# Performance work log

Measured on AMD Instinct MI355X. Metric: run time of the kernel, lower is better.

## Reference

```python
import jax, jax.numpy as jnp
import numpy as np

EMB = 1024
HID = 4 * EMB
HEADS = 16
HEAD_DIM = EMB // HEADS


def gelu_tanh(x):
    c = jnp.sqrt(jnp.asarray(2.0 / jnp.pi, x.dtype))
    return 0.5 * x * (1.0 + jnp.tanh(c * (x + 0.044715 * x ** 3)))


def layernorm(x, scale, shift, eps=1e-5):
    mean = jnp.mean(x, axis=-1, keepdims=True)
    var = jnp.var(x, axis=-1, keepdims=True)
    return scale * (x - mean) / jnp.sqrt(var + eps) + shift


def setup_inputs() -> dict:
    key = jax.random.key(0)
    ks = jax.random.split(key, 12)
    s = 0.02
    return {
        "x": jax.random.normal(ks[0], (2, 2048, EMB), jnp.float32),
        "Wq": jax.random.normal(ks[1], (EMB, EMB), jnp.float32) * s,
        "Wk": jax.random.normal(ks[2], (EMB, EMB), jnp.float32) * s,
        "Wv": jax.random.normal(ks[3], (EMB, EMB), jnp.float32) * s,
        "Wo": jax.random.normal(ks[4], (EMB, EMB), jnp.float32) * s,
        "bo": jnp.zeros((EMB,), jnp.float32),
        "W1": jax.random.normal(ks[5], (EMB, HID), jnp.float32) * s,
        "b1": jnp.zeros((HID,), jnp.float32),
        "W2": jax.random.normal(ks[6], (HID, EMB), jnp.float32) * s,
        "b2": jnp.zeros((EMB,), jnp.float32),
        "ln1_scale": jnp.ones((EMB,), jnp.float32),
        "ln1_shift": jnp.zeros((EMB,), jnp.float32),
        "ln2_scale": jnp.ones((EMB,), jnp.float32),
        "ln2_shift": jnp.zeros((EMB,), jnp.float32),
    }


def reference(x, Wq, Wk, Wv, Wo, bo, W1, b1, W2, b2,
              ln1_scale, ln1_shift, ln2_scale, ln2_shift):
    B, S, D = x.shape

    # pre-norm attention + residual
    h = layernorm(x, ln1_scale, ln1_shift)
    q = (h @ Wq).reshape(B, S, HEADS, HEAD_DIM).transpose(0, 2, 1, 3)  # bhsd
    k = (h @ Wk).reshape(B, S, HEADS, HEAD_DIM).transpose(0, 2, 1, 3)
    v = (h @ Wv).reshape(B, S, HEADS, HEAD_DIM).transpose(0, 2, 1, 3)

    scores = jnp.einsum("bhqd,bhkd->bhqk", q, k)
    causal = jnp.tril(jnp.ones((S, S), bool))
    scores = jnp.where(causal, scores, -jnp.inf)
    attn = jax.nn.softmax(scores / jnp.sqrt(jnp.asarray(HEAD_DIM, x.dtype)), axis=-1)
    ctx = jnp.einsum("bhqk,bhkd->bhqd", attn, v)
    ctx = ctx.transpose(0, 2, 1, 3).reshape(B, S, D)
    x = x + (ctx @ Wo + bo)

    # pre-norm FFN + residual
    h = layernorm(x, ln2_scale, ln2_shift)
    h = gelu_tanh(h @ W1 + b1) @ W2 + b2
    return x + h
```

## Files before the change

kernel.cpp:

```cpp
#include <hip/hip_runtime.h>
#include <hip/hip_bf16.h>
#include <stdint.h>

#define B_   2
#define S_   2048
#define D_   1024
#define H_   16
#define DH_  64
#define HID_ 4096
#define M_   4096

typedef __bf16 bf16x8 __attribute__((ext_vector_type(8)));
typedef float  f32x4  __attribute__((ext_vector_type(4)));
typedef float  f32x16 __attribute__((ext_vector_type(16)));
typedef uint32_t u32x4v __attribute__((ext_vector_type(4)));

typedef const uint32_t __attribute__((address_space(1))) u32g;
typedef uint32_t       __attribute__((address_space(3))) u32l;

#define SCL2K_ 0.18033688011112042f

__device__ __forceinline__ uint16_t f2bf(float f) {
  uint32_t u = __builtin_bit_cast(uint32_t, f);
  u += 0x7FFFu + ((u >> 16) & 1u);
  return (uint16_t)(u >> 16);
}

__device__ __forceinline__ float bf2f(uint16_t u) {
  return __builtin_bit_cast(float, (uint32_t)u << 16);
}

__device__ __forceinline__ void gload_lds16(const void* g, void* l) {
  __builtin_amdgcn_global_load_lds((u32g*)g, (u32l*)l, 16, 0, 0);
}

__device__ __forceinline__ const bf16x8* lds8p(const uint16_t* base, int row,
                                               int cole) {
  int byt = (cole * 2) ^ ((row & 7) << 4);
  return reinterpret_cast<const bf16x8*>(base + row * 64 + (byt >> 1));
}

__device__ __forceinline__ const bf16x8* lds8p32(const uint16_t* base, int row,
                                                 int cole) {
  int byt = (cole * 2) ^ ((row & 7) << 4) ^ ((row & 8) << 2);
  return reinterpret_cast<const bf16x8*>(base + row * 64 + (byt >> 1));
}

__device__ __forceinline__ uint32_t cvtpk_bf16(float lo, float hi) {
  uint32_t d;
  asm("v_cvt_pk_bf16_f32 %0, %1, %2" : "=v"(d) : "v"(lo), "v"(hi));
  return d;
}
__device__ __forceinline__ void pl32swap(uint32_t& a, uint32_t& b) {
  asm volatile("v_permlane32_swap_b32 %0, %1" : "+v"(a), "+v"(b));
}

__global__ void prep_k(const float* __restrict__ Wq, const float* __restrict__ Wk,
                       const float* __restrict__ Wv, const float* __restrict__ Wo,
                       const float* __restrict__ W1, const float* __restrict__ W2,
                       uint16_t* __restrict__ WQKVT, uint16_t* __restrict__ WOT,
                       uint16_t* __restrict__ W1T, uint16_t* __restrict__ W2T,
                       const float* __restrict__ x, const float* __restrict__ sc,
                       const float* __restrict__ sh, uint16_t* __restrict__ lnout) {
  int idx = blockIdx.x;
  int tx = threadIdx.x, ty = threadIdx.y;
  if (idx >= 12288) {
    int row = idx - 12288;
    int t = ty * 32 + tx;
    float4 v = reinterpret_cast<const float4*>(x + (size_t)row * D_)[t];
    float s = v.x + v.y + v.z + v.w;
    float ss = v.x * v.x + v.y * v.y + v.z * v.z + v.w * v.w;
#pragma unroll
    for (int off = 32; off >= 1; off >>= 1) {
      s += __shfl_xor(s, off);
      ss += __shfl_xor(ss, off);
    }
    __shared__ float red[8];
    int wid = t >> 6, lane = t & 63;
    if (lane == 0) { red[wid] = s; red[wid + 4] = ss; }
    __syncthreads();
    s = red[0] + red[1] + red[2] + red[3];
    ss = red[4] + red[5] + red[6] + red[7];
    float mean = s * (1.0f / D_);
    float var = ss * (1.0f / D_) - mean * mean;
    float rstd = rsqrtf(var + 1e-5f);
    float4 g = reinterpret_cast<const float4*>(sc)[t];
    float4 b = reinterpret_cast<const float4*>(sh)[t];
    ushort4 o;
    o.x = f2bf(g.x * (v.x - mean) * rstd + b.x);
    o.y = f2bf(g.y * (v.y - mean) * rstd + b.y);
    o.z = f2bf(g.z * (v.z - mean) * rstd + b.z);
    o.w = f2bf(g.w * (v.w - mean) * rstd + b.w);
    reinterpret_cast<ushort4*>(lnout + (size_t)row * D_)[t] = o;
    return;
  }
  __shared__ float tile[32][33];
  const float* W;
  uint16_t* WT;
  int K, N, within;
  if (idx < 4096) {
    int which = idx >> 10;
    within = idx & 1023;
    W = (which == 0) ? Wq : (which == 1) ? Wk : (which == 2) ? Wv : Wo;
    WT = (which == 3) ? WOT : WQKVT + (size_t)which * 1024 * 1024;
    K = 1024; N = 1024;
  } else if (idx < 8192) {
    within = idx - 4096; W = W1; WT = W1T; K = 1024; N = 4096;
  } else {
    within = idx - 8192; W = W2; WT = W2T; K = 4096; N = 1024;
  }
  int nb = N >> 5;
  int n0 = (within % nb) * 32, k0 = (within / nb) * 32;
#pragma unroll
  for (int i = 0; i < 4; ++i)
    tile[ty + i * 8][tx] = W[(size_t)(k0 + ty + i * 8) * N + n0 + tx];
  __syncthreads();
#pragma unroll
  for (int i = 0; i < 4; ++i)
    WT[(size_t)(n0 + ty + i * 8) * K + k0 + tx] = f2bf(tile[tx][ty + i * 8]);
}

__global__ __launch_bounds__(256) void ln_k(const float* __restrict__ x,
                                            const float* __restrict__ sc,
                                            const float* __restrict__ sh,
                                            uint16_t* __restrict__ out) {
  int row = blockIdx.x;
  int t = threadIdx.x;
  float4 v = reinterpret_cast<const float4*>(x + (size_t)row * D_)[t];
  float s = v.x + v.y + v.z + v.w;
  float ss = v.x * v.x + v.y * v.y + v.z * v.z + v.w * v.w;
#pragma unroll
  for (int off = 32; off >= 1; off >>= 1) {
    s += __shfl_xor(s, off);
    ss += __shfl_xor(ss, off);
  }
  __shared__ float red[8];
  int wid = t >> 6, lane = t & 63;
  if (lane == 0) { red[wid] = s; red[wid + 4] = ss; }
  __syncthreads();
  s = red[0] + red[1] + red[2] + red[3];
  ss = red[4] + red[5] + red[6] + red[7];
  float mean = s * (1.0f / D_);
  float var = ss * (1.0f / D_) - mean * mean;
  float rstd = rsqrtf(var + 1e-5f);
  float4 g = reinterpret_cast<const float4*>(sc)[t];
  float4 b = reinterpret_cast<const float4*>(sh)[t];
  ushort4 o;
  o.x = f2bf(g.x * (v.x - mean) * rstd + b.x);
  o.y = f2bf(g.y * (v.y - mean) * rstd + b.y);
  o.z = f2bf(g.z * (v.z - mean) * rstd + b.z);
  o.w = f2bf(g.w * (v.w - mean) * rstd + b.w);
  reinterpret_cast<ushort4*>(out + (size_t)row * D_)[t] = o;
}

__global__ __launch_bounds__(256) void reduce4_k(
    const uint16_t* __restrict__ P0, const uint16_t* __restrict__ P1,
    const uint16_t* __restrict__ P2, const uint16_t* __restrict__ P3,
    const float* __restrict__ resid, const float* __restrict__ bias,
    float* __restrict__ out) {
  int row = blockIdx.x, t = threadIdx.x;
  size_t base = (size_t)row * D_ + t * 4;
  float4 r = *reinterpret_cast<const float4*>(resid + base);
  float4 b = reinterpret_cast<const float4*>(bias)[t];
  ushort4 u0 = *reinterpret_cast<const ushort4*>(P0 + base);
  ushort4 u1 = *reinterpret_cast<const ushort4*>(P1 + base);
  ushort4 u2 = *reinterpret_cast<const ushort4*>(P2 + base);
  ushort4 u3 = *reinterpret_cast<const ushort4*>(P3 + base);
  float4 o;
  o.x = r.x + b.x + bf2f(u0.x) + bf2f(u1.x) + bf2f(u2.x) + bf2f(u3.x);
  o.y = r.y + b.y + bf2f(u0.y) + bf2f(u1.y) + bf2f(u2.y) + bf2f(u3.y);
  o.z = r.z + b.z + bf2f(u0.z) + bf2f(u1.z) + bf2f(u2.z) + bf2f(u3.z);
  o.w = r.w + b.w + bf2f(u0.w) + bf2f(u1.w) + bf2f(u2.w) + bf2f(u3.w);
  *reinterpret_cast<float4*>(out + base) = o;
}

template <int EPI>
__global__ __launch_bounds__(512, 2) void gemm8(
    const uint16_t* __restrict__ A, const uint16_t* __restrict__ BT,
    void* __restrict__ Cout, const float* __restrict__ bias,
    uint16_t* __restrict__ P0, uint16_t* __restrict__ P1,
    uint16_t* __restrict__ P2, uint16_t* __restrict__ P3,
    int M, int N, int K) {
  __shared__ uint16_t As[2][2][128 * 64];
  __shared__ uint16_t Bs[2][2][128 * 64];
  int t = threadIdx.x;
  int lane = t & 63, wid = t >> 6;
  int wm = wid >> 2, wn = wid & 3;
  int l15 = lane & 15, lk8 = (lane >> 4) * 8, lr4 = (lane >> 4) * 4;
  int gx = gridDim.x;
  int nwg = gx * gridDim.y;
  int bid = blockIdx.y * gx + blockIdx.x;
  int swz = (bid & 7) * (nwg >> 3) + (bid >> 3);
  int bx = swz % gx, by = swz / gx;
  int m0 = by * 256, n0 = bx * 256;
  int ksz = K / gridDim.z;
  int kbeg = blockIdx.z * ksz;
  int NT = ksz >> 6;

  int r0 = t >> 3, slot0 = t & 7;
  int scol = (slot0 ^ (r0 & 7)) * 8;

  auto STAGE_A = [&](int kt, int half, int buf) {
    const uint16_t* src =
        A + (size_t)(m0 + half * 128 + r0) * K + kbeg + kt * 64 + scol;
    uint16_t* dst = &As[buf][half][t * 8];
    gload_lds16(src, dst);
    gload_lds16(src + (size_t)64 * K, dst + 4096);
  };
  auto STAGE_B = [&](int kt, int half, int buf) {
    const uint16_t* src =
        BT + (size_t)(n0 + half * 128 + r0) * K + kbeg + kt * 64 + scol;
    uint16_t* dst = &Bs[buf][half][t * 8];
    gload_lds16(src, dst);
    gload_lds16(src + (size_t)64 * K, dst + 4096);
  };

  bf16x8 a[4][2], b[2][2];
  auto LDA = [&](int buf, int mh) {
#pragma unroll
    for (int j = 0; j < 4; ++j)
#pragma unroll
      for (int kk = 0; kk < 2; ++kk)
        a[j][kk] = *lds8p(As[buf][mh], wm * 64 + j * 16 + l15, kk * 32 + lk8);
  };
  auto LDB = [&](int buf, int nh) {
#pragma unroll
    for (int jj = 0; jj < 2; ++jj)
#pragma unroll
      for (int kk = 0; kk < 2; ++kk)
        b[jj][kk] = *lds8p(Bs[buf][nh], wn * 32 + jj * 16 + l15, kk * 32 + lk8);
  };

  f32x4 acc[8][4] = {};
  auto MM = [&](int mh, int nh) {
    __builtin_amdgcn_s_setprio(1);
#pragma unroll
    for (int kk = 0; kk < 2; ++kk)
#pragma unroll
      for (int j = 0; j < 4; ++j)
#pragma unroll
        for (int jj = 0; jj < 2; ++jj)
          acc[mh * 4 + j][nh * 2 + jj] = __builtin_amdgcn_mfma_f32_16x16x32_bf16(
              a[j][kk], b[jj][kk], acc[mh * 4 + j][nh * 2 + jj], 0, 0, 0);
    __builtin_amdgcn_s_setprio(0);
  };
  auto BAR = [&]() { __builtin_amdgcn_s_barrier(); };

  STAGE_A(0, 0, 0);
  STAGE_B(0, 1, 0);
  STAGE_B(0, 0, 0);
  STAGE_A(0, 1, 0);
  STAGE_A(1, 0, 1);
  STAGE_B(1, 1, 1);
  asm volatile("s_waitcnt vmcnt(4)" ::: "memory");
  BAR();

  for (int T = 0; T < NT; ++T) {
    int cur = T & 1;
    LDA(cur, 0);
    LDB(cur, 0);
    if (T + 1 < NT) STAGE_B(T + 1, 0, cur ^ 1);
    BAR();
    MM(0, 0);
    BAR();
    LDB(cur, 1);
    if (T + 1 < NT) STAGE_A(T + 1, 1, cur ^ 1);
    BAR();
    MM(0, 1);
    BAR();
    LDA(cur, 1);
    if (T + 2 < NT) STAGE_A(T + 2, 0, cur);
    BAR();
    MM(1, 1);
    BAR();
    LDB(cur, 0);
    if (T + 2 < NT) STAGE_B(T + 2, 1, cur);
    BAR();
    MM(1, 0);
    if (T + 1 < NT) {
      if (T == NT - 2) {
        asm volatile("s_waitcnt vmcnt(0)" ::: "memory");
      } else {
        asm volatile("s_waitcnt vmcnt(4)" ::: "memory");
      }
    }
    BAR();
  }

  uint16_t* Pz = nullptr;
  if constexpr (EPI == 3) {
    int z = blockIdx.z;
    Pz = (z == 0) ? P0 : (z == 1) ? P1 : (z == 2) ? P2 : P3;
  }
#pragma unroll
  for (int mi = 0; mi < 8; ++mi) {
#pragma unroll
    for (int ni = 0; ni < 4; ++ni) {
      int gm0 = m0 + (mi >> 2) * 128 + wm * 64 + (mi & 3) * 16 + lr4;
      int gn = n0 + (ni >> 1) * 128 + wn * 32 + (ni & 1) * 16 + l15;
      if constexpr (EPI == 0) {
        int which = gn >> 10, nc = gn & 1023;
        int h = nc >> 6, dh = nc & 63;
        int bb = gm0 >> 11, s0 = gm0 & 2047;
        if (which == 2) {
          ushort4 vs;
          vs.x = f2bf(acc[mi][ni][0]);
          vs.y = f2bf(acc[mi][ni][1]);
          vs.z = f2bf(acc[mi][ni][2]);
          vs.w = f2bf(acc[mi][ni][3]);
          uint16_t* VTb = P0;
          *reinterpret_cast<ushort4*>(
              VTb + ((size_t)(bb * 16 + h) * 64 + dh) * S_ + s0) = vs;
        } else {
#pragma unroll
          for (int rr = 0; rr < 4; ++rr) {
            float v = acc[mi][ni][rr];
            if (which == 1) v *= SCL2K_;
            ((uint16_t*)Cout)[((size_t)which * 32 + bb * 16 + h) * (S_ * 64) +
                              (size_t)(s0 + rr) * 64 + dh] = f2bf(v);
          }
        }
      } else {
#pragma unroll
        for (int rr = 0; rr < 4; ++rr) {
          int gm = gm0 + rr;
          float v = acc[mi][ni][rr];
          if constexpr (EPI == 2) {
            float u = v + bias[gn];
            float y = 0.7978845608028654f * (u + 0.044715f * u * u * u);
            float e = __expf(2.0f * y);
            float th = 1.0f - 2.0f / (e + 1.0f);
            ((uint16_t*)Cout)[(size_t)gm * N + gn] = f2bf(0.5f * u * (1.0f + th));
          } else {
            Pz[(size_t)gm * N + gn] = f2bf(v);
          }
        }
      }
    }
  }
}

template <int EPI>
__global__ __launch_bounds__(256) void gemm_bt(
    const uint16_t* __restrict__ A, const uint16_t* __restrict__ BT,
    void* __restrict__ Cout, const float* __restrict__ bias,
    const float* __restrict__ resid, int M, int N, int K) {
  __shared__ uint16_t Asm_[128 * 64];
  __shared__ uint16_t Bsm_[128 * 64];
  int t = threadIdx.x;
  int lane = t & 63, wid = t >> 6;
  int wr = wid >> 1, wc = wid & 1;
  int nwg = gridDim.x * gridDim.y;
  int bid = blockIdx.y * gridDim.x + blockIdx.x;
  int swz = (bid & 7) * (nwg >> 3) + (bid >> 3);
  int bx = swz % gridDim.x, by = swz / gridDim.x;
  int m0 = by * 128, n0 = bx * 128;
  int l15 = lane & 15, lk8 = (lane >> 4) * 8;
  f32x4 acc[4][4] = {};

  auto STAGE = [&](int k0) {
#pragma unroll
    for (int it = 0; it < 4; ++it) {
      int idx = it * 256 + t;
      int r = idx >> 3, slot = idx & 7;
      int c = (slot ^ (r & 7)) * 8;
      gload_lds16(A + (size_t)(m0 + r) * K + k0 + c, &Asm_[idx * 8]);
      gload_lds16(BT + (size_t)(n0 + r) * K + k0 + c, &Bsm_[idx * 8]);
    }
  };

  int niter = K >> 6;
  for (int ki = 0; ki < niter; ++ki) {
    __syncthreads();
    STAGE(ki * 64);
    __syncthreads();
#pragma unroll
    for (int kk = 0; kk < 2; ++kk) {
      bf16x8 a[4], b[4];
#pragma unroll
      for (int mi = 0; mi < 4; ++mi)
        a[mi] = *lds8p(Asm_, wr * 64 + mi * 16 + l15, kk * 32 + lk8);
#pragma unroll
      for (int ni = 0; ni < 4; ++ni)
        b[ni] = *lds8p(Bsm_, wc * 64 + ni * 16 + l15, kk * 32 + lk8);
#pragma unroll
      for (int mi = 0; mi < 4; ++mi)
#pragma unroll
        for (int ni = 0; ni < 4; ++ni)
          acc[mi][ni] = __builtin_amdgcn_mfma_f32_16x16x32_bf16(
              a[mi], b[ni], acc[mi][ni], 0, 0, 0);
    }
  }
  int lr4 = (lane >> 4) * 4;
#pragma unroll
  for (int mi = 0; mi < 4; ++mi) {
#pragma unroll
    for (int ni = 0; ni < 4; ++ni) {
#pragma unroll
      for (int r = 0; r < 4; ++r) {
        int gm = m0 + wr * 64 + mi * 16 + lr4 + r;
        int gn = n0 + wc * 64 + ni * 16 + l15;
        float v = acc[mi][ni][r];
        if constexpr (EPI == 1) {
          ((float*)Cout)[(size_t)gm * N + gn] =
              resid[(size_t)gm * N + gn] + v + bias[gn];
        }
      }
    }
  }
}

__global__ __launch_bounds__(64) void attn32s_k(const uint16_t* __restrict__ Q,
                                                const uint16_t* __restrict__ Kv,
                                                const uint16_t* __restrict__ VT,
                                                uint16_t* __restrict__ Obuf,
                                                float* __restrict__ ML) {
  __shared__ uint16_t Ksm[2][32 * 64];
  __shared__ uint16_t Vsm[2][32 * 64];
  int bid = blockIdx.x;
  int bh = bid & 31;
  int s = (bid >> 5) % 3;
  int qt = 63 - bid / 96;
  int lane = threadIdx.x;
  int l31 = lane & 31, lh = lane >> 5;
  int nkt = qt + 1;
  int chunk = (nkt + 2) / 3;
  int t0 = s * chunk, t1 = min(nkt, t0 + chunk);
  int pb = (qt * 32 + bh) * 3 + s;

  f32x16 o0 = {}, o1 = {};
  float mrow = -3.0e38f, lsum = 0.0f;

  auto STAGE = [&](int k0, int bufi) {
#pragma unroll
    for (int c = 0; c < 4; ++c) {
      int idx = c * 64 + lane;
      int r = idx >> 3, sl = idx & 7;
      int slp = sl ^ (r & 7) ^ ((r & 8) >> 2);
      gload_lds16(Kv + ((size_t)bh * S_ + k0 + r) * 64 + slp * 8,
                  &Ksm[bufi][idx * 8]);
      int dh = 2 * r + (slp >> 2), ko = (slp & 3) * 8;
      gload_lds16(VT + ((size_t)bh * 64 + dh) * S_ + k0 + ko,
                  &Vsm[bufi][idx * 8]);
    }
  };

  if (t0 < t1) {
    int qbase = qt * 32;
    bf16x8 qf[4];
#pragma unroll
    for (int dk = 0; dk < 4; ++dk)
      qf[dk] = *reinterpret_cast<const bf16x8*>(
          Q + ((size_t)bh * S_ + qbase + l31) * 64 + dk * 16 + lh * 8);

    int buf = 0;
    STAGE(t0 * 32, 0);
    for (int t = t0; t < t1; ++t) {
      if (t + 1 < t1) {
        STAGE((t + 1) * 32, buf ^ 1);
        asm volatile("s_waitcnt vmcnt(8)" ::: "memory");
      } else {
        asm volatile("s_waitcnt vmcnt(0)" ::: "memory");
      }
      __builtin_amdgcn_sched_barrier(0);
      f32x16 Sf = {};
      __builtin_amdgcn_s_setprio(1);
#pragma unroll
      for (int dk = 0; dk < 4; ++dk) {
        bf16x8 kf = *lds8p32(Ksm[buf], l31, dk * 16 + lh * 8);
        Sf = __builtin_amdgcn_mfma_f32_32x32x16_bf16(kf, qf[dk], Sf, 0, 0, 0);
      }
      __builtin_amdgcn_s_setprio(0);
      float sv[16];
      if (t == qt) {
#pragma unroll
        for (int rr = 0; rr < 16; ++rr) {
          int koff = (rr & 3) + 8 * (rr >> 2) + 4 * lh;
          sv[rr] = (koff <= l31) ? Sf[rr] : -3.0e38f;
        }
      } else {
#pragma unroll
        for (int rr = 0; rr < 16; ++rr) sv[rr] = Sf[rr];
      }
      float mt16 = sv[0];
#pragma unroll
      for (int rr = 1; rr < 16; ++rr) mt16 = fmaxf(mt16, sv[rr]);
      if (__any(mt16 > mrow + 8.0f)) {
        float mt = mt16;
#pragma unroll
        for (int off = 32; off >= 1; off >>= 1)
          mt = fmaxf(mt, __shfl_xor(mt, off));
        mt = fmaxf(mt, mrow);
        float fac = __builtin_amdgcn_exp2f(mrow - mt);
        mrow = mt;
        lsum *= fac;
#pragma unroll
        for (int rr = 0; rr < 16; ++rr) { o0[rr] *= fac; o1[rr] *= fac; }
      }
      float pv[16];
#pragma unroll
      for (int rr = 0; rr < 16; ++rr) {
        pv[rr] = __builtin_amdgcn_exp2f(sv[rr] - mrow);
        lsum += pv[rr];
      }
      uint32_t a0 = cvtpk_bf16(pv[0], pv[1]), b0 = cvtpk_bf16(pv[4], pv[5]);
      pl32swap(a0, b0);
      uint32_t a1 = cvtpk_bf16(pv[2], pv[3]), b1 = cvtpk_bf16(pv[6], pv[7]);
      pl32swap(a1, b1);
      u32x4v w0 = {a0, a1, b0, b1};
      bf16x8 pa0 = __builtin_bit_cast(bf16x8, w0);
      uint32_t a2 = cvtpk_bf16(pv[8], pv[9]), b2 = cvtpk_bf16(pv[12], pv[13]);
      pl32swap(a2, b2);
      uint32_t a3 = cvtpk_bf16(pv[10], pv[11]), b3 = cvtpk_bf16(pv[14], pv[15]);
      pl32swap(a3, b3);
      u32x4v w1 = {a2, a3, b2, b3};
      bf16x8 pa1 = __builtin_bit_cast(bf16x8, w1);
      int vrow = l31 >> 1, vcb = (l31 & 1) * 32 + lh * 8;
      __builtin_amdgcn_s_setprio(1);
      bf16x8 v00 = *lds8p32(Vsm[buf], vrow, vcb);
      o0 = __builtin_amdgcn_mfma_f32_32x32x16_bf16(pa0, v00, o0, 0, 0, 0);
      bf16x8 v01 = *lds8p32(Vsm[buf], vrow, vcb + 16);
      o0 = __builtin_amdgcn_mfma_f32_32x32x16_bf16(pa1, v01, o0, 0, 0, 0);
      bf16x8 v10 = *lds8p32(Vsm[buf], 16 + vrow, vcb);
      o1 = __builtin_amdgcn_mfma_f32_32x32x16_bf16(pa0, v10, o1, 0, 0, 0);
      bf16x8 v11 = *lds8p32(Vsm[buf], 16 + vrow, vcb + 16);
      o1 = __builtin_amdgcn_mfma_f32_32x32x16_bf16(pa1, v11, o1, 0, 0, 0);
      __builtin_amdgcn_s_setprio(0);
      buf ^= 1;
    }
    lsum += __shfl_xor(lsum, 32);
  }

  if (lane < 32) {
    ML[(size_t)pb * 64 + l31 * 2] = mrow;
    ML[(size_t)pb * 64 + l31 * 2 + 1] = lsum;
  }
#pragma unroll
  for (int rr = 0; rr < 16; ++rr) {
    int srow = (rr & 3) + 8 * (rr >> 2) + 4 * lh;
    size_t base = (size_t)pb * 2048 + srow * 64;
    Obuf[base + l31] = f2bf(o0[rr]);
    Obuf[base + 32 + l31] = f2bf(o1[rr]);
  }
}

__global__ __launch_bounds__(64) void attncomb_k(const uint16_t* __restrict__ Obuf,
                                                 const float* __restrict__ ML,
                                                 uint16_t* __restrict__ ctx) {
  int blk = blockIdx.x;
  int qt = blk >> 5, bh = blk & 31;
  int lane = threadIdx.x;
  int q = lane >> 1, half = lane & 1;
  size_t pb0 = (size_t)blk * 3;
  float m0 = ML[pb0 * 64 + q * 2], l0 = ML[pb0 * 64 + q * 2 + 1];
  float m1 = ML[(pb0 + 1) * 64 + q * 2], l1 = ML[(pb0 + 1) * 64 + q * 2 + 1];
  float m2 = ML[(pb0 + 2) * 64 + q * 2], l2 = ML[(pb0 + 2) * 64 + q * 2 + 1];
  float m = fmaxf(fmaxf(m0, m1), m2);
  float w0 = __builtin_amdgcn_exp2f(m0 - m);
  float w1 = __builtin_amdgcn_exp2f(m1 - m);
  float w2 = __builtin_amdgcn_exp2f(m2 - m);
  float invL = 1.0f / (l0 * w0 + l1 * w1 + l2 * w2);
  int b_ = bh >> 4, h_ = bh & 15;
  int srow = qt * 32 + q;
  size_t ib = pb0 * 2048 + q * 64 + half * 32;
  size_t ob = ((size_t)(b_ * S_ + srow)) * D_ + h_ * 64 + half * 32;
#pragma unroll
  for (int i = 0; i < 8; ++i) {
    ushort4 u0 = *reinterpret_cast<const ushort4*>(Obuf + ib + i * 4);
    ushort4 u1 = *reinterpret_cast<const ushort4*>(Obuf + 2048 + ib + i * 4);
    ushort4 u2 = *reinterpret_cast<const ushort4*>(Obuf + 4096 + ib + i * 4);
    ushort4 o;
    o.x = f2bf((bf2f(u0.x) * w0 + bf2f(u1.x) * w1 + bf2f(u2.x) * w2) * invL);
    o.y = f2bf((bf2f(u0.y) * w0 + bf2f(u1.y) * w1 + bf2f(u2.y) * w2) * invL);
    o.z = f2bf((bf2f(u0.z) * w0 + bf2f(u1.z) * w1 + bf2f(u2.z) * w2) * invL);
    o.w = f2bf((bf2f(u0.w) * w0 + bf2f(u1.w) * w1 + bf2f(u2.w) * w2) * invL);
    *reinterpret_cast<ushort4*>(ctx + ob + i * 4) = o;
  }
}

extern "C" void kernel_launch(void* const* d_in, const int* in_sizes, int n_in,
                              void* d_out, int out_size, void* d_ws, size_t ws_size,
                              hipStream_t stream) {
  const float* x    = (const float*)d_in[0];
  const float* Wq   = (const float*)d_in[1];
  const float* Wk   = (const float*)d_in[2];
  const float* Wv   = (const float*)d_in[3];
  const float* Wo   = (const float*)d_in[4];
  const float* bo   = (const float*)d_in[5];
  const float* W1   = (const float*)d_in[6];
  const float* b1   = (const float*)d_in[7];
  const float* W2   = (const float*)d_in[8];
  const float* b2   = (const float*)d_in[9];
  const float* ln1s = (const float*)d_in[10];
  const float* ln1b = (const float*)d_in[11];
  const float* ln2s = (const float*)d_in[12];
  const float* ln2b = (const float*)d_in[13];
  float* out = (float*)d_out;
  char* ws = (char*)d_ws;

  const size_t MB = 1024 * 1024;
  uint16_t* WQKVT = (uint16_t*)(ws + 0);
  uint16_t* WOT   = (uint16_t*)(ws + 6 * MB);
  uint16_t* W1T   = (uint16_t*)(ws + 8 * MB);
  uint16_t* W2T   = (uint16_t*)(ws + 16 * MB);
  uint16_t* H1    = (uint16_t*)(ws + 24 * MB);
  float*    X1    = (float*)(ws + 32 * MB);
  uint16_t* QKV   = (uint16_t*)(ws + 48 * MB);
  uint16_t* VTb   = (uint16_t*)(ws + 72 * MB);
  uint16_t* CTX   = (uint16_t*)(ws + 80 * MB);
  uint16_t* FFH   = (uint16_t*)(ws + 48 * MB);
  uint16_t* AOB   = (uint16_t*)(ws + 24 * MB);
  float*    AML   = (float*)(ws + 0);
  uint16_t* SP0   = (uint16_t*)(ws + 0);
  uint16_t* SP1   = (uint16_t*)(ws + 8 * MB);
  uint16_t* SP2   = (uint16_t*)(ws + 24 * MB);
  uint16_t* SP3   = (uint16_t*)(ws + 80 * MB);

  dim3 b32x8(32, 8);
  prep_k<<<dim3(16384), b32x8, 0, stream>>>(Wq, Wk, Wv, Wo, W1, W2,
                                            WQKVT, WOT, W1T, W2T,
                                            x, ln1s, ln1b, H1);
  gemm8<0><<<dim3(12, 16), 512, 0, stream>>>(H1, WQKVT, QKV, nullptr,
                                             VTb, nullptr, nullptr, nullptr,
                                             M_, 3072, 1024);
  const uint16_t* Qp = QKV;
  const uint16_t* Kp = QKV + (size_t)32 * S_ * 64;
  attn32s_k<<<dim3(6144), 64, 0, stream>>>(Qp, Kp, VTb, AOB, AML);
  attncomb_k<<<dim3(2048), 64, 0, stream>>>(AOB, AML, CTX);
  gemm_bt<1><<<dim3(8, 32), 256, 0, stream>>>(CTX, WOT, X1, bo, x, M_, 1024, 1024);
  ln_k<<<M_, 256, 0, stream>>>(X1, ln2s, ln2b, H1);
  gemm8<2><<<dim3(16, 16), 512, 0, stream>>>(H1, W1T, FFH, b1,
                                             nullptr, nullptr, nullptr, nullptr,
                                             M_, 4096, 1024);
  gemm8<3><<<dim3(4, 16, 4), 512, 0, stream>>>(FFH, W2T, nullptr, nullptr,
                                               SP0, SP1, SP2, SP3,
                                               M_, 1024, 4096);
  reduce4_k<<<M_, 256, 0, stream>>>(SP0, SP1, SP2, SP3, X1, b2, out);
}
```

Baseline: 234.0 us.

## Double-buffer GEMM register fragments to overlap LDS reads with MFMA

The bf16 GEMM kernel now keeps two sets of A and B register fragments. The next half-tile's LDS reads are issued right before the MFMA block that uses the current fragments, and the first fragments of the next K-tile are prefetched after the loop's final barrier. It also reuses the B fragment for the last quadrant instead of reloading it from LDS. The K-split size is hardcoded to 1024 so the tile loop can be fully unrolled. The extra live fragment registers add pressure on top of the 128-float accumulator under a 512x2 launch bound, which risks spills or lower occupancy. The hardcoded K chunk assumes every launch uses K/gridDim.z == 1024.

```diff
diff --git a/kernel.cpp b/kernel.cpp
--- a/kernel.cpp
+++ b/kernel.cpp
@@ -181,6 +181,8 @@
     uint16_t* __restrict__ P0, uint16_t* __restrict__ P1,
     uint16_t* __restrict__ P2, uint16_t* __restrict__ P3,
     int M, int N, int K) {
+  constexpr int KSZ = 1024;
+  constexpr int NT = KSZ >> 6;
   __shared__ uint16_t As[2][2][128 * 64];
   __shared__ uint16_t Bs[2][2][128 * 64];
   int t = threadIdx.x;
@@ -193,9 +195,7 @@
   int swz = (bid & 7) * (nwg >> 3) + (bid >> 3);
   int bx = swz % gx, by = swz / gx;
   int m0 = by * 256, n0 = bx * 256;
-  int ksz = K / gridDim.z;
-  int kbeg = blockIdx.z * ksz;
-  int NT = ksz >> 6;
+  int kbeg = blockIdx.z * KSZ;
 
   int r0 = t >> 3, slot0 = t & 7;
   int scol = (slot0 ^ (r0 & 7)) * 8;
@@ -215,24 +215,24 @@
     gload_lds16(src + (size_t)64 * K, dst + 4096);
   };
 
-  bf16x8 a[4][2], b[2][2];
-  auto LDA = [&](int buf, int mh) {
+  bf16x8 aA[4][2], aB[4][2], bA[2][2], bB[2][2];
+  auto LDAf = [&](bf16x8 (&dst)[4][2], int buf, int mh) {
 #pragma unroll
     for (int j = 0; j < 4; ++j)
 #pragma unroll
       for (int kk = 0; kk < 2; ++kk)
-        a[j][kk] = *lds8p(As[buf][mh], wm * 64 + j * 16 + l15, kk * 32 + lk8);
+        dst[j][kk] = *lds8p(As[buf][mh], wm * 64 + j * 16 + l15, kk * 32 + lk8);
   };
-  auto LDB = [&](int buf, int nh) {
+  auto LDBf = [&](bf16x8 (&dst)[2][2], int buf, int nh) {
 #pragma unroll
     for (int jj = 0; jj < 2; ++jj)
 #pragma unroll
       for (int kk = 0; kk < 2; ++kk)
-        b[jj][kk] = *lds8p(Bs[buf][nh], wn * 32 + jj * 16 + l15, kk * 32 + lk8);
+        dst[jj][kk] = *lds8p(Bs[buf][nh], wn * 32 + jj * 16 + l15, kk * 32 + lk8);
   };
 
   f32x4 acc[8][4] = {};
-  auto MM = [&](int mh, int nh) {
+  auto MMf = [&](bf16x8 (&a)[4][2], bf16x8 (&b)[2][2], int mh, int nh) {
     __builtin_amdgcn_s_setprio(1);
 #pragma unroll
     for (int kk = 0; kk < 2; ++kk)
@@ -254,29 +254,29 @@
   STAGE_B(1, 1, 1);
   asm volatile("s_waitcnt vmcnt(4)" ::: "memory");
   BAR();
-
+  LDAf(aA, 0, 0);
+  LDBf(bA, 0, 0);
+
+#pragma unroll
   for (int T = 0; T < NT; ++T) {
     int cur = T & 1;
-    LDA(cur, 0);
-    LDB(cur, 0);
     if (T + 1 < NT) STAGE_B(T + 1, 0, cur ^ 1);
     BAR();
-    MM(0, 0);
-    BAR();
-    LDB(cur, 1);
+    LDBf(bB, cur, 1);
+    MMf(aA, bA, 0, 0);
+    BAR();
     if (T + 1 < NT) STAGE_A(T + 1, 1, cur ^ 1);
     BAR();
-    MM(0, 1);
-    BAR();
-    LDA(cur, 1);
+    LDAf(aB, cur, 1);
+    MMf(aA, bB, 0, 1);
+    BAR();
     if (T + 2 < NT) STAGE_A(T + 2, 0, cur);
     BAR();
-    MM(1, 1);
-    BAR();
-    LDB(cur, 0);
+    MMf(aB, bB, 1, 1);
+    BAR();
     if (T + 2 < NT) STAGE_B(T + 2, 1, cur);
     BAR();
-    MM(1, 0);
+    MMf(aB, bA, 1, 0);
     if (T + 1 < NT) {
       if (T == NT - 2) {
         asm volatile("s_waitcnt vmcnt(0)" ::: "memory");
@@ -285,6 +285,10 @@
       }
     }
     BAR();
+    if (T + 1 < NT) {
+      LDAf(aA, cur ^ 1, 0);
+      LDBf(bA, cur ^ 1, 0);
+    }
   }
 
   uint16_t* Pz = nullptr;
```

Measured after the change: 231.2 us. About the same (-1.2%).
